# Optimization experiments

Measured on AMD Instinct MI355X. Metric: run time of the kernel, lower is better.

The kernel has to match this reference:

```python
import jax, jax.numpy as jnp
import numpy as np

B, N, C_IN = 8, 4096, 64
M, K = 1024, 32          # npoints, knn k
C_COV, C_OUT = 64, 128   # mlp_cov out channels, mlp_f out channels


def setup_inputs() -> dict:
    key = jax.random.key(0)
    k0, k1, k2, k3 = jax.random.split(key, 4)
    return {
        "f": jax.random.normal(k0, (B, C_IN, N), jnp.float32),
        "xyz": jax.random.normal(k1, (B, N, 3), jnp.float32),
        "W_cov": jax.random.normal(k2, (C_COV, 9), jnp.float32) * 0.1,
        "b_cov": jnp.zeros((C_COV,), jnp.float32),
        "W_f": jax.random.normal(k3, (C_OUT, C_IN + C_COV), jnp.float32) * 0.1,
        "b_f": jnp.zeros((C_OUT,), jnp.float32),
    }


def _fps_single(pts):
    """Farthest point sampling on one cloud [N,3] -> [M] indices (start at 0)."""
    n = pts.shape[0]

    def step(carry, _):
        dists, far = carry
        d = jnp.sum((pts - pts[far]) ** 2, axis=-1)   # [N]
        dists = jnp.minimum(dists, d)
        nxt = jnp.argmax(dists).astype(jnp.int32)
        return (dists, nxt), far

    init = (jnp.full((n,), 1e10, pts.dtype), jnp.int32(0))
    _, idxs = jax.lax.scan(step, init, None, length=M)
    return idxs  # [M]


def reference(f, xyz, W_cov, b_cov, W_f, b_f):
    # FPS: [B, M] sampled indices, gather new centroids [B, M, 3]
    sample_idx = jax.vmap(_fps_single)(xyz)
    xyz_new = jnp.take_along_axis(xyz, sample_idx[:, :, None], axis=1)  # [B,M,3]

    # Brute-force KNN: squared distances [B, M, N], take k smallest
    d2 = jnp.sum((xyz_new[:, :, None, :] - xyz[:, None, :, :]) ** 2, axis=-1)
    _, idx = jax.lax.top_k(-d2, K)  # idx: [B, M, K]

    # Group features [B, C, M, K] and max-pool over neighbors -> [B, C, M]
    grouped = jax.vmap(lambda fb, ib: fb[:, ib])(f, idx)
    f_max = grouped.max(axis=-1)

    # Local covariance of neighbor coordinates -> [B, 9, M]
    nbr = jax.vmap(lambda pb, ib: pb[ib])(xyz, idx)          # [B, M, K, 3]
    centered = nbr - nbr.mean(axis=2, keepdims=True)
    covm = jnp.einsum('bmki,bmkj->bmij', centered, centered) / K  # [B,M,3,3]
    cov9 = covm.reshape(B, M, 9).transpose(0, 2, 1)          # [B, 9, M]

    # mlp_cov: 1x1 conv (9 -> C_COV) + ReLU
    f_cov = jax.nn.relu(jnp.einsum('co,bom->bcm', W_cov, cov9) + b_cov[None, :, None])

    # concat on channel dim, mlp_f: 1x1 conv (C_IN+C_COV -> C_OUT) + ReLU
    f_cat = jnp.concatenate([f_max, f_cov], axis=1)          # [B, 128, M]
    out = jax.nn.relu(jnp.einsum('co,bom->bcm', W_f, f_cat) + b_f[None, :, None])
    return (out, xyz_new)
```

## Files before the change

kernel.cpp:

```cpp
#include <hip/hip_runtime.h>
#include <hip/hip_bf16.h>
#include <stdint.h>

#define BATCH 8
#define NPTS  4096
#define CIN   64
#define MPTS  1024
#define KNN   32
#define CCOV  64
#define COUT  128
#define CCAP  1024

typedef unsigned long long u64;
typedef unsigned int u32;

__global__ void k_transpose(const float* __restrict__ f, float* __restrict__ fT) {
    __shared__ float tile[64][65];
    int b  = blockIdx.y;
    int n0 = blockIdx.x * 64;
    int tx = threadIdx.x & 63;
    int ty = threadIdx.x >> 6;
#pragma unroll
    for (int r = 0; r < 16; ++r) {
        int c = r * 4 + ty;
        tile[c][tx] = f[((size_t)b * CIN + c) * NPTS + n0 + tx];
    }
    __syncthreads();
#pragma unroll
    for (int r = 0; r < 16; ++r) {
        int n = r * 4 + ty;
        fT[((size_t)b * NPTS + n0 + n) * CIN + tx] = tile[tx][n];
    }
}

template <int CTRL>
__device__ __forceinline__ float dpp_step_max(float x) {
    int xi = __float_as_int(x);
    int yi = __builtin_amdgcn_update_dpp(xi, xi, CTRL, 0xF, 0xF, false);
    return fmaxf(x, __int_as_float(yi));
}
__device__ __forceinline__ float wave_max_dpp(float x) {
    x = dpp_step_max<0x111>(x);
    x = dpp_step_max<0x112>(x);
    x = dpp_step_max<0x114>(x);
    x = dpp_step_max<0x118>(x);
    x = dpp_step_max<0x142>(x);
    x = dpp_step_max<0x143>(x);
    return __int_as_float(__builtin_amdgcn_readlane(__float_as_int(x), 63));
}

__launch_bounds__(256, 1)
__global__ void k_fps(const float* __restrict__ xyz, float* __restrict__ xyz_new) {
    __shared__ float sx[NPTS], sy[NPTS], sz[NPTS];
    __shared__ int   sel[MPTS];
    __shared__ __align__(16) u64 wkeys[2][4];
    __shared__ u64 wkey2[2];
    __shared__ int rcnt[2];
    __shared__ int rcand[2][32];

    int b    = blockIdx.x;
    int tid  = threadIdx.x;
    int lane = tid & 63, wid = tid >> 6;
    const float* xb = xyz + (size_t)b * NPTS * 3;
    float px[16], py[16], pz[16], dist[16];
#pragma unroll
    for (int j = 0; j < 16; ++j) {
        int i = tid + 256 * j;
        px[j] = xb[i * 3 + 0];
        py[j] = xb[i * 3 + 1];
        pz[j] = xb[i * 3 + 2];
        sx[i] = px[j]; sy[i] = py[j]; sz[i] = pz[j];
        dist[j] = 1e30f;
    }
    __syncthreads();

    int far = 0;

    for (int m = 0; m < MPTS; ++m) {
        int p = m & 1;
        float fx = sx[far], fy = sy[far], fz = sz[far];
        if (tid == 0) {
            sel[m] = far;
            rcnt[p] = 0; wkey2[p] = 0;
        }
        float lmax = 0.f;
#pragma unroll
        for (int j = 0; j < 16; ++j) {
            float dx = px[j] - fx, dy = py[j] - fy, dz = pz[j] - fz;
            float d  = fmaf(dx, dx, fmaf(dy, dy, dz * dz));
            dist[j] = fminf(dist[j], d);
            lmax = fmaxf(lmax, dist[j]);
        }
        float wm = wave_max_dpp(lmax);
        float wthresh = wm * (1.0f - 4e-6f);
        int cw = 0;
        u32 idxw = 0xFFFu;
#pragma unroll
        for (int j = 0; j < 16; ++j) {
            u64 bj = __ballot(dist[j] >= wthresh);
            cw += (int)__popcll(bj);
            if (bj) idxw = (u32)(wid * 64 + (int)__builtin_ctzll(bj) + 256 * j);
        }
        u64 key = ((u64)__float_as_uint(wm) << 32) |
                  ((u64)(u32)(cw > 255 ? 255 : cw) << 12) | (u64)idxw;
        if (lane == 0) wkeys[p][wid] = key;
        __syncthreads();

        ulonglong2 q0 = *(const ulonglong2*)&wkeys[p][0];
        ulonglong2 q1 = *(const ulonglong2*)&wkeys[p][2];
        u64 ka = q0.x > q0.y ? q0.x : q0.y;
        u64 kb = q1.x > q1.y ? q1.x : q1.y;
        u64 kmax = ka > kb ? ka : kb;
        float gmax = __uint_as_float((u32)(kmax >> 32));
        float gthresh = gmax * (1.0f - 4e-6f);
        int tot = 0;
        {
            u64 ks[4] = {q0.x, q0.y, q1.x, q1.y};
#pragma unroll
            for (int w = 0; w < 4; ++w) {
                float wmw = __uint_as_float((u32)(ks[w] >> 32));
                if (wmw >= gthresh) tot += (int)((ks[w] >> 12) & 0xFFull);
            }
        }

        if (tot == 1) {
            far = (int)(kmax & 0xFFFull);
        } else {
#pragma unroll
            for (int j = 0; j < 16; ++j) {
                if (dist[j] >= gthresh) {
                    int pos = atomicAdd(&rcnt[p], 1);
                    if (pos < 32) rcand[p][pos] = tid + 256 * j;
                }
            }
            __syncthreads();
            int nc = rcnt[p] < 32 ? rcnt[p] : 32;
            for (int c = wid; c < nc; c += 4) {
                int i = rcand[p][c];
                double cx = (double)sx[i], cy = (double)sy[i], cz = (double)sz[i];
                double dmin = 1e10;
                for (int t = lane; t <= m; t += 64) {
                    int s = sel[t];
                    double ddx = __dsub_rn(cx, (double)sx[s]);
                    double ddy = __dsub_rn(cy, (double)sy[s]);
                    double ddz = __dsub_rn(cz, (double)sz[s]);
                    double d64 = __dadd_rn(__dadd_rn(__dmul_rn(ddx, ddx),
                                                     __dmul_rn(ddy, ddy)),
                                           __dmul_rn(ddz, ddz));
                    dmin = fmin(dmin, d64);
                }
#pragma unroll
                for (int off = 32; off; off >>= 1)
                    dmin = fmin(dmin, __shfl_xor(dmin, off));
                if (lane == 0)
                    atomicMax(&wkey2[p],
                              ((u64)__double_as_longlong(dmin) & ~0xFFFull) |
                              (u64)((~(u32)i) & 0xFFFu));
            }
            __syncthreads();
            far = (int)((~(u32)wkey2[p]) & 0xFFFu);
        }
    }

    __syncthreads();
    float* xout = xyz_new + (size_t)b * MPTS * 3;
    for (int mm = tid; mm < MPTS; mm += 256) {
        int s = sel[mm];
        xout[mm * 3 + 0] = sx[s];
        xout[mm * 3 + 1] = sy[s];
        xout[mm * 3 + 2] = sz[s];
    }
}

__launch_bounds__(64)
__global__ void k_knn(const float* __restrict__ xyz, const float* __restrict__ xyz_new,
                      const float* __restrict__ fT, const float* __restrict__ Wcov,
                      const float* __restrict__ bcov, float* __restrict__ fcat) {
    __shared__ u32 cidx[CCAP];
    __shared__ u64 kbuf[CCAP];
    __shared__ int sknn[KNN];
    __shared__ int cnt;

    int q = blockIdx.x;
    int b = q >> 10, m = q & 1023;
    int lane = threadIdx.x;
    const float* xb = xyz + (size_t)b * NPTS * 3;

    float cxf = xyz_new[((size_t)b * MPTS + m) * 3 + 0];
    float cyf = xyz_new[((size_t)b * MPTS + m) * 3 + 1];
    float czf = xyz_new[((size_t)b * MPTS + m) * 3 + 2];
    double cx = (double)cxf, cy = (double)cyf, cz = (double)czf;

    if (lane == 0) cnt = 0;

    float d[64];
    float lmin = 1e30f;
#pragma unroll
    for (int t = 0; t < 64; ++t) {
        int i = lane + 64 * t;
        float dx = cxf - xb[i * 3 + 0];
        float dy = cyf - xb[i * 3 + 1];
        float dz = czf - xb[i * 3 + 2];
        d[t] = fmaf(dx, dx, fmaf(dy, dy, dz * dz));
        lmin = fminf(lmin, d[t]);
    }
    float c0  = wave_max_dpp(lmin);
    float cut = c0 * (1.0f + 4e-6f);
    __syncthreads();

#pragma unroll
    for (int t = 0; t < 64; ++t) {
        if (d[t] <= cut) {
            int pos = atomicAdd(&cnt, 1);
            if (pos < CCAP) cidx[pos] = (u32)(lane + 64 * t);
        }
    }
    __syncthreads();
    int n0 = cnt;

    if (n0 <= CCAP) {
        for (int c = lane; c < n0; c += 64) {
            int i = (int)cidx[c];
            double dx = __dsub_rn(cx, (double)xb[i * 3 + 0]);
            double dy = __dsub_rn(cy, (double)xb[i * 3 + 1]);
            double dz = __dsub_rn(cz, (double)xb[i * 3 + 2]);
            double d2 = __dadd_rn(__dadd_rn(__dmul_rn(dx, dx), __dmul_rn(dy, dy)),
                                  __dmul_rn(dz, dz));
            kbuf[c] = ((u64)__double_as_longlong(d2) & ~0xFFFull) | (u64)i;
        }
        u64 thr = 0;
        for (int it = 0; it < KNN; ++it) {
            u64 best = ~0ull;
            for (int c = lane; c < n0; c += 64) {
                u64 v = kbuf[c];
                if (v >= thr && v < best) best = v;
            }
#pragma unroll
            for (int off = 1; off < 64; off <<= 1) {
                u64 o = __shfl_xor(best, off);
                if (o < best) best = o;
            }
            if (lane == 0) sknn[it] = (int)(best & 0xFFFull);
            thr = best + 1;
        }
    } else {
        u64 thr = 0;
        for (int it = 0; it < KNN; ++it) {
            u64 best = ~0ull;
#pragma unroll 4
            for (int t = 0; t < 64; ++t) {
                int i = lane + 64 * t;
                double dx = __dsub_rn(cx, (double)xb[i * 3 + 0]);
                double dy = __dsub_rn(cy, (double)xb[i * 3 + 1]);
                double dz = __dsub_rn(cz, (double)xb[i * 3 + 2]);
                double d2 = __dadd_rn(__dadd_rn(__dmul_rn(dx, dx), __dmul_rn(dy, dy)),
                                      __dmul_rn(dz, dz));
                u64 v = ((u64)__double_as_longlong(d2) & ~0xFFFull) | (u64)i;
                if (v >= thr && v < best) best = v;
            }
#pragma unroll
            for (int off = 1; off < 64; off <<= 1) {
                u64 o = __shfl_xor(best, off);
                if (o < best) best = o;
            }
            if (lane == 0) sknn[it] = (int)(best & 0xFFFull);
            thr = best + 1;
        }
    }
    __syncthreads();

    int nk = sknn[lane & 31];
    float nx = xb[nk * 3 + 0], ny = xb[nk * 3 + 1], nz = xb[nk * 3 + 2];
    float sxs = nx, sys = ny, szs = nz;
#pragma unroll
    for (int off = 1; off < 64; off <<= 1) {
        sxs += __shfl_xor(sxs, off);
        sys += __shfl_xor(sys, off);
        szs += __shfl_xor(szs, off);
    }
    float mx = sxs * (1.f / 64.f), my = sys * (1.f / 64.f), mz = szs * (1.f / 64.f);
    float ux = nx - mx, uy = ny - my, uz = nz - mz;
    float pxx = ux * ux, pxy = ux * uy, pxz = ux * uz;
    float pyy = uy * uy, pyz = uy * uz, pzz = uz * uz;
#pragma unroll
    for (int off = 1; off < 64; off <<= 1) {
        pxx += __shfl_xor(pxx, off);
        pxy += __shfl_xor(pxy, off);
        pxz += __shfl_xor(pxz, off);
        pyy += __shfl_xor(pyy, off);
        pyz += __shfl_xor(pyz, off);
        pzz += __shfl_xor(pzz, off);
    }
    const float inv = 1.f / 64.f;
    float c9[9];
    c9[0] = pxx * inv; c9[1] = pxy * inv; c9[2] = pxz * inv;
    c9[3] = pxy * inv; c9[4] = pyy * inv; c9[5] = pyz * inv;
    c9[6] = pxz * inv; c9[7] = pyz * inv; c9[8] = pzz * inv;

    float acc = bcov[lane];
#pragma unroll
    for (int j = 0; j < 9; ++j) acc = fmaf(Wcov[lane * 9 + j], c9[j], acc);
    float fcov = fmaxf(acc, 0.f);

    float fm = -1e30f;
#pragma unroll
    for (int kk = 0; kk < KNN; ++kk) {
        int ni = sknn[kk];
        fm = fmaxf(fm, fT[((size_t)b * NPTS + ni) * CIN + lane]);
    }

    float* dst = fcat + (size_t)q * (CIN + CCOV);
    dst[lane]       = fm;
    dst[CIN + lane] = fcov;
}

__global__ void k_mlp(const float* __restrict__ fcat, const float* __restrict__ Wf,
                      const float* __restrict__ bf, float* __restrict__ out) {
    __shared__ float tile[32][132];
    int b  = blockIdx.y;
    int m0 = blockIdx.x * 32;
    int tid = threadIdx.x;
    const float4* src = (const float4*)(fcat + ((size_t)b * MPTS + m0) * 128);
#pragma unroll
    for (int r = 0; r < 4; ++r) {
        int e  = tid + 256 * r;
        int mm = e >> 5;
        int c4 = e & 31;
        float4 v = src[e];
        *(float4*)&tile[mm][c4 * 4] = v;
    }
    __syncthreads();

    int m   = tid & 31;
    int cog = tid >> 5;
    float acc[16];
#pragma unroll
    for (int j = 0; j < 16; ++j) acc[j] = bf[cog * 16 + j];

    for (int c4 = 0; c4 < 32; ++c4) {
        float4 fv = *(const float4*)&tile[m][c4 * 4];
#pragma unroll
        for (int j = 0; j < 16; ++j) {
            int co = cog * 16 + j;
            float4 wv = ((const float4*)(Wf + (size_t)co * 128))[c4];
            acc[j] = fmaf(wv.x, fv.x, acc[j]);
            acc[j] = fmaf(wv.y, fv.y, acc[j]);
            acc[j] = fmaf(wv.z, fv.z, acc[j]);
            acc[j] = fmaf(wv.w, fv.w, acc[j]);
        }
    }
#pragma unroll
    for (int j = 0; j < 16; ++j) {
        int co = cog * 16 + j;
        out[((size_t)b * COUT + co) * MPTS + m0 + m] = fmaxf(acc[j], 0.f);
    }
}

extern "C" void kernel_launch(void* const* d_in, const int* in_sizes, int n_in,
                              void* d_out, int out_size, void* d_ws, size_t ws_size,
                              hipStream_t stream) {
    const float* f    = (const float*)d_in[0];
    const float* xyz  = (const float*)d_in[1];
    const float* Wcov = (const float*)d_in[2];
    const float* bcov = (const float*)d_in[3];
    const float* Wf   = (const float*)d_in[4];
    const float* bf   = (const float*)d_in[5];

    float* out     = (float*)d_out;
    float* xyz_new = out + (size_t)BATCH * COUT * MPTS;

    float* fT   = (float*)d_ws;
    float* fcat = fT + (size_t)BATCH * NPTS * CIN;

    k_transpose<<<dim3(64, BATCH), 256, 0, stream>>>(f, fT);
    k_fps<<<BATCH, 256, 0, stream>>>(xyz, xyz_new);
    k_knn<<<BATCH * MPTS, 64, 0, stream>>>(xyz, xyz_new, fT, Wcov, bcov, fcat);
    k_mlp<<<dim3(MPTS / 32, BATCH), 256, 0, stream>>>(fcat, Wf, bf, out);
}
```

Before: 1.219 ms.

## Run FPS with a single wavefront per batch to drop block barriers

The farthest-point-sampling kernel moves from four wavefronts per batch to one wavefront that holds 64 points per lane in registers. The cross-wave key exchange and the per-iteration __syncthreads are removed, so argmax selection comes from the wave reduction plus ballots alone. The cost is four times more serial work per lane, 256 live registers of point data per lane, and a tie-break pass that now loops over candidates serially in one wave.

Result: slower. 2.540 ms (+108.4%).

```diff
diff --git a/kernel.cpp b/kernel.cpp
--- a/kernel.cpp
+++ b/kernel.cpp
@@ -49,23 +49,21 @@
     return __int_as_float(__builtin_amdgcn_readlane(__float_as_int(x), 63));
 }
 
-__launch_bounds__(256, 1)
+__launch_bounds__(64, 1)
 __global__ void k_fps(const float* __restrict__ xyz, float* __restrict__ xyz_new) {
     __shared__ float sx[NPTS], sy[NPTS], sz[NPTS];
     __shared__ int   sel[MPTS];
-    __shared__ __align__(16) u64 wkeys[2][4];
-    __shared__ u64 wkey2[2];
-    __shared__ int rcnt[2];
-    __shared__ int rcand[2][32];
+    __shared__ u64 wkey2;
+    __shared__ int rcnt;
+    __shared__ int rcand[64];
 
     int b    = blockIdx.x;
-    int tid  = threadIdx.x;
-    int lane = tid & 63, wid = tid >> 6;
+    int lane = threadIdx.x;
     const float* xb = xyz + (size_t)b * NPTS * 3;
-    float px[16], py[16], pz[16], dist[16];
-#pragma unroll
-    for (int j = 0; j < 16; ++j) {
-        int i = tid + 256 * j;
+    float px[64], py[64], pz[64], dist[64];
+#pragma unroll
+    for (int j = 0; j < 64; ++j) {
+        int i = lane + 64 * j;
         px[j] = xb[i * 3 + 0];
         py[j] = xb[i * 3 + 1];
         pz[j] = xb[i * 3 + 2];
@@ -77,66 +75,45 @@
     int far = 0;
 
     for (int m = 0; m < MPTS; ++m) {
-        int p = m & 1;
         float fx = sx[far], fy = sy[far], fz = sz[far];
-        if (tid == 0) {
-            sel[m] = far;
-            rcnt[p] = 0; wkey2[p] = 0;
-        }
+        if (lane == 0) sel[m] = far;
         float lmax = 0.f;
 #pragma unroll
-        for (int j = 0; j < 16; ++j) {
+        for (int j = 0; j < 64; ++j) {
             float dx = px[j] - fx, dy = py[j] - fy, dz = pz[j] - fz;
             float d  = fmaf(dx, dx, fmaf(dy, dy, dz * dz));
             dist[j] = fminf(dist[j], d);
             lmax = fmaxf(lmax, dist[j]);
         }
         float wm = wave_max_dpp(lmax);
-        float wthresh = wm * (1.0f - 4e-6f);
-        int cw = 0;
-        u32 idxw = 0xFFFu;
-#pragma unroll
-        for (int j = 0; j < 16; ++j) {
-            u64 bj = __ballot(dist[j] >= wthresh);
-            cw += (int)__popcll(bj);
-            if (bj) idxw = (u32)(wid * 64 + (int)__builtin_ctzll(bj) + 256 * j);
-        }
-        u64 key = ((u64)__float_as_uint(wm) << 32) |
-                  ((u64)(u32)(cw > 255 ? 255 : cw) << 12) | (u64)idxw;
-        if (lane == 0) wkeys[p][wid] = key;
-        __syncthreads();
-
-        ulonglong2 q0 = *(const ulonglong2*)&wkeys[p][0];
-        ulonglong2 q1 = *(const ulonglong2*)&wkeys[p][2];
-        u64 ka = q0.x > q0.y ? q0.x : q0.y;
-        u64 kb = q1.x > q1.y ? q1.x : q1.y;
-        u64 kmax = ka > kb ? ka : kb;
-        float gmax = __uint_as_float((u32)(kmax >> 32));
-        float gthresh = gmax * (1.0f - 4e-6f);
+        float gthresh = wm * (1.0f - 4e-6f);
+
         int tot = 0;
-        {
-            u64 ks[4] = {q0.x, q0.y, q1.x, q1.y};
-#pragma unroll
-            for (int w = 0; w < 4; ++w) {
-                float wmw = __uint_as_float((u32)(ks[w] >> 32));
-                if (wmw >= gthresh) tot += (int)((ks[w] >> 12) & 0xFFull);
-            }
-        }
-
+        int widx = 0;
+#pragma unroll
+        for (int j = 0; j < 64; ++j) {
+            u64 bj = __ballot(dist[j] >= gthresh);
+            if (bj) {
+                tot += (int)__popcll(bj);
+                widx = (int)__builtin_ctzll(bj) + 64 * j;
+            }
+        }
         if (tot == 1) {
-            far = (int)(kmax & 0xFFFull);
+            far = widx;
         } else {
-#pragma unroll
-            for (int j = 0; j < 16; ++j) {
+            if (lane == 0) { rcnt = 0; wkey2 = 0; }
+            __syncthreads();
+#pragma unroll
+            for (int j = 0; j < 64; ++j) {
                 if (dist[j] >= gthresh) {
-                    int pos = atomicAdd(&rcnt[p], 1);
-                    if (pos < 32) rcand[p][pos] = tid + 256 * j;
+                    int pos = atomicAdd(&rcnt, 1);
+                    if (pos < 64) rcand[pos] = lane + 64 * j;
                 }
             }
             __syncthreads();
-            int nc = rcnt[p] < 32 ? rcnt[p] : 32;
-            for (int c = wid; c < nc; c += 4) {
-                int i = rcand[p][c];
+            int nc = rcnt < 64 ? rcnt : 64;
+            for (int c = 0; c < nc; ++c) {
+                int i = rcand[c];
                 double cx = (double)sx[i], cy = (double)sy[i], cz = (double)sz[i];
                 double dmin = 1e10;
                 for (int t = lane; t <= m; t += 64) {
@@ -153,18 +130,18 @@
                 for (int off = 32; off; off >>= 1)
                     dmin = fmin(dmin, __shfl_xor(dmin, off));
                 if (lane == 0)
-                    atomicMax(&wkey2[p],
+                    atomicMax(&wkey2,
                               ((u64)__double_as_longlong(dmin) & ~0xFFFull) |
                               (u64)((~(u32)i) & 0xFFFu));
             }
             __syncthreads();
-            far = (int)((~(u32)wkey2[p]) & 0xFFFu);
+            far = (int)((~(u32)wkey2) & 0xFFFu);
         }
     }
 
     __syncthreads();
     float* xout = xyz_new + (size_t)b * MPTS * 3;
-    for (int mm = tid; mm < MPTS; mm += 256) {
+    for (int mm = lane; mm < MPTS; mm += 64) {
         int s = sel[mm];
         xout[mm * 3 + 0] = sx[s];
         xout[mm * 3 + 1] = sy[s];
@@ -373,7 +350,7 @@
     float* fcat = fT + (size_t)BATCH * NPTS * CIN;
 
     k_transpose<<<dim3(64, BATCH), 256, 0, stream>>>(f, fT);
-    k_fps<<<BATCH, 256, 0, stream>>>(xyz, xyz_new);
+    k_fps<<<BATCH, 64, 0, stream>>>(xyz, xyz_new);
     k_knn<<<BATCH * MPTS, 64, 0, stream>>>(xyz, xyz_new, fT, Wcov, bcov, fcat);
     k_mlp<<<dim3(MPTS / 32, BATCH), 256, 0, stream>>>(fcat, Wf, bf, out);
 }
```
